# Kernel optimization log

Hardware: AMD Instinct MI355X
Metric: run time of the kernel (lower is better)

Reference implementation:

```python
import math
import jax, jax.numpy as jnp
import numpy as np

# ---- SLAYER neuron / simulation constants (from config) ----
THETA = 10.0      # spike threshold
TAU_SR = 10.0     # PSP (SRM) kernel time constant
TAU_REF = 1.0     # refractory kernel time constant
TS = 1.0          # simulation time step
T_SAMPLE = 500    # number of time bins
B, N_IN, N_HID, N_OUT = 64, 1024, 1024, 10


def _alpha_kernel(tau, mult, eps=0.01):
    """slayer _calculateAlphaKernel: mult * t/tau * exp(1 - t/tau), truncated."""
    vals = []
    t = 0.0
    while t < T_SAMPLE:
        v = mult * t / tau * math.exp(1.0 - t / tau)
        if abs(v) < eps and t > tau:
            break
        vals.append(v)
        t += TS
    return np.asarray(vals, np.float32)

SRM_KERNEL = jnp.asarray(_alpha_kernel(TAU_SR, 1.0))            # [K]
REF_KERNEL = jnp.asarray(_alpha_kernel(TAU_REF, -2.0 * THETA))  # [Kr], REF_KERNEL[0] == 0


def dense(x, W):
    # per-timestep fully-connected layer (slayer.dense == 1x1x1 conv3d, no bias)
    # x: [B, Nin, T], W: [Nout, Nin] -> [B, Nout, T]
    return jnp.einsum('oi,bit->bot', W, x)


def psp(x):
    # causal temporal convolution with the SRM kernel: out[t] = Ts * sum_k srm[k] * x[t-k]
    Bx, N, T = x.shape
    K = SRM_KERNEL.shape[0]
    k = SRM_KERNEL[::-1].reshape(1, 1, K).astype(x.dtype)  # flip -> true convolution
    y = jax.lax.conv_general_dilated(
        x.reshape(Bx * N, 1, T), k, (1,), [(K - 1, 0)],
        dimension_numbers=('NCH', 'OIH', 'NCH'))
    return y.reshape(Bx, N, T) * TS


def spike_impl(u_in):
    # sequential LIF thresholding with refractory feedback (slayer spike kernel)
    # u_in: [B, N, T] membrane drive; returns (spikes, membrane) both [B, N, T]
    Kr = REF_KERNEL.shape[0]
    # buf[j] is the refractory contribution arriving at step t+j; new spike at t
    # contributes REF_KERNEL[j] at t+j (REF_KERNEL[0]==0), i.e. shifted kernel into buf.
    refk = jnp.concatenate([REF_KERNEL[1:], jnp.zeros((1,), u_in.dtype)]).astype(u_in.dtype)
    buf0 = jnp.zeros(u_in.shape[:-1] + (Kr,), u_in.dtype)

    def step(buf, u_t):
        u = u_t + buf[..., 0]                              # membrane at time t
        s = (u >= THETA).astype(u_in.dtype) / TS           # spike (amplitude 1/Ts)
        buf = jnp.concatenate([buf[..., 1:], jnp.zeros_like(buf[..., :1])], axis=-1)
        buf = buf + s[..., None] * refk
        return buf, (s, u)

    _, (s, u) = jax.lax.scan(step, buf0, jnp.moveaxis(u_in, -1, 0))
    return jnp.moveaxis(s, 0, -1), jnp.moveaxis(u, 0, -1)


def setup_inputs() -> dict:
    key = jax.random.key(0)
    k1, k2, k3 = jax.random.split(key, 3)
    spike_input = (jax.random.uniform(k1, (B, N_IN, T_SAMPLE)) < 0.05).astype(jnp.float32)
    W1 = jax.random.normal(k2, (N_HID, N_IN), jnp.float32) * 0.3
    W2 = jax.random.normal(k3, (N_OUT, N_HID), jnp.float32) * 0.3
    return {"spike_input": spike_input, "W1": W1, "W2": W2}


def reference(spike_input, W1, W2):
    s1, _ = spike_impl(psp(dense(spike_input, W1)))
    s2, _ = spike_impl(psp(dense(s1, W2)))
    return s2
```

## Files before the change

kernel.cpp:

```cpp
#include <hip/hip_runtime.h>
#include <stdint.h>
#include <math.h>

#define T_SIM 500
#define NB    64
#define NIN   1024
#define NHID  1024
#define NOUT  10
#define KSRM  77
#define CHUNK 32
#define TT5   12
#define NT5   42
#define RINGN 104
#define NGW   16

__device__ __forceinline__ double srm_tap(int k) {
  double u = (double)k / 10.0;
  double v = u * exp(1.0 - u);
  return (double)(float)v;
}
__device__ __forceinline__ double ref_tap(int j) {
  double v = (-20.0 * (double)j) * exp(1.0 - (double)j);
  return (double)(float)v;
}

__global__ __launch_bounds__(64)
void k_pack(const float* __restrict__ x, unsigned long long* __restrict__ bits) {
  const int b = blockIdx.x, ig = blockIdx.y, tc = blockIdx.z;
  const int lane = threadIdx.x;
  const float* xr = x + ((size_t)b * NIN + ig * 64 + lane) * T_SIM;
  const int t0 = tc * 100;
  for (int t = t0; t < t0 + 100; t += 4) {
    const float4 v = *(const float4*)(xr + t);
    unsigned long long m0 = __ballot(v.x > 0.5f);
    unsigned long long m1 = __ballot(v.y > 0.5f);
    unsigned long long m2 = __ballot(v.z > 0.5f);
    unsigned long long m3 = __ballot(v.w > 0.5f);
    if (lane == 0) {
      unsigned long long* w = bits + (size_t)(b * T_SIM + t) * 16 + ig;
      w[0] = m0; w[16] = m1; w[32] = m2; w[48] = m3;
    }
  }
}

__global__ __launch_bounds__(256)
void k_transpose(const float* __restrict__ W1, float* __restrict__ W1T) {
  __shared__ float tile[64][65];
  const int bo = blockIdx.x * 64, bi = blockIdx.y * 64;
  for (int k = threadIdx.x; k < 4096; k += 256) {
    int r = k >> 6, c = k & 63;
    tile[r][c] = W1[(size_t)(bo + r) * NIN + bi + c];
  }
  __syncthreads();
  for (int k = threadIdx.x; k < 4096; k += 256) {
    int r = k >> 6, c = k & 63;
    W1T[(size_t)(bi + r) * NHID + bo + c] = tile[c][r];
  }
}

__global__ __launch_bounds__(128)
void k_dense1(const uint32_t* __restrict__ bits, const float* __restrict__ W1T,
              double* __restrict__ a1c, int col_base) {
  __shared__ int list[NIN];
  __shared__ int nact_s;
  const int col_loc = blockIdx.x;
  const int tid = threadIdx.x;
  if (tid < 32) {
    uint32_t w = bits[(size_t)(col_base + col_loc) * 32 + tid];
    int c = __popc(w);
    int p = c;
#pragma unroll
    for (int d = 1; d < 32; d <<= 1) {
      int q = __shfl_up(p, d);
      if (tid >= d) p += q;
    }
    int excl = p - c;
    while (w) {
      const int j = __ffs(w) - 1;
      w &= w - 1;
      list[excl++] = tid * 32 + j;
    }
    if (tid == 31) nact_s = excl;
  }
  __syncthreads();
  const int n = nact_s;
  const int o = blockIdx.y * 512 + tid * 4;
  double ax[4] = {0,0,0,0}, ay[4] = {0,0,0,0};
  double az[4] = {0,0,0,0}, aw[4] = {0,0,0,0};
  float4 L[8];
  int g = 0;
  if (n >= 8) {
#pragma unroll
    for (int r = 0; r < 8; ++r)
      L[r] = *(const float4*)(W1T + (size_t)list[r] * NHID + o);
    for (g = 0; g + 16 <= n; g += 8) {
      float4 Nb[8];
#pragma unroll
      for (int r = 0; r < 8; ++r)
        Nb[r] = *(const float4*)(W1T + (size_t)list[g + 8 + r] * NHID + o);
#pragma unroll
      for (int r = 0; r < 8; ++r) {
        const int s = r & 3;
        ax[s] += (double)L[r].x; ay[s] += (double)L[r].y;
        az[s] += (double)L[r].z; aw[s] += (double)L[r].w;
      }
#pragma unroll
      for (int r = 0; r < 8; ++r) L[r] = Nb[r];
    }
#pragma unroll
    for (int r = 0; r < 8; ++r) {
      const int s = r & 3;
      ax[s] += (double)L[r].x; ay[s] += (double)L[r].y;
      az[s] += (double)L[r].z; aw[s] += (double)L[r].w;
    }
    g += 8;
  }
  for (; g < n; ++g) {
    const float4 wv = *(const float4*)(W1T + (size_t)list[g] * NHID + o);
    const int s = g & 3;
    ax[s] += (double)wv.x; ay[s] += (double)wv.y;
    az[s] += (double)wv.z; aw[s] += (double)wv.w;
  }
  double* dst = a1c + (size_t)col_loc * NHID + o;
  __builtin_nontemporal_store((ax[0] + ax[1]) + (ax[2] + ax[3]), dst + 0);
  __builtin_nontemporal_store((ay[0] + ay[1]) + (ay[2] + ay[3]), dst + 1);
  __builtin_nontemporal_store((az[0] + az[1]) + (az[2] + az[3]), dst + 2);
  __builtin_nontemporal_store((aw[0] + aw[1]) + (aw[2] + aw[3]), dst + 3);
}

__global__ __launch_bounds__(256)
void k_ps1(const double* __restrict__ a1c, uint16_t* __restrict__ s1h,
           int b_base) {
  __shared__ double S[RINGN * NGW];
  __shared__ double Yp[2][4][TT5 * NGW];
  __shared__ double TB[80];
  const int ng = blockIdx.x, b_loc = blockIdx.y;
  const int tid = threadIdx.x;
  const double* __restrict__ abase = a1c + (size_t)b_loc * T_SIM * NHID + ng * NGW;
  uint16_t* __restrict__ sbase = s1h + (size_t)(b_base + b_loc) * T_SIM * 64 + ng;

  if (tid < 80) TB[tid] = (tid <= 76) ? srm_tap(tid) : 0.0;
  for (int i = tid; i < RINGN * NGW; i += 256) S[i] = 0.0;
  __syncthreads();
  for (int id = tid; id < TT5 * NGW; id += 256) {
    const int r = id >> 4, nn = id & 15;
    S[r * NGW + nn] = abase[(size_t)r * NHID + nn];
  }

  const bool isFIR = (tid < 192);
  const int g   = tid / 48;
  const int rem = tid - g * 48;
  const int q   = rem >> 4;
  const int n   = rem & 15;
  double tap[20];
  __syncthreads();
  if (isFIR) {
#pragma unroll
    for (int j = 0; j < 20; ++j) tap[j] = TB[20 * g + j];
  }
  double refk[11];
#pragma unroll
  for (int j = 1; j <= 10; ++j) refk[j] = ref_tap(j);
  uint32_t smask = 0;

  for (int k = 0; k < NT5; ++k) {
    const int t0 = k * TT5;
    const int tv = (T_SIM - t0 < TT5) ? (T_SIM - t0) : TT5;
    const int t0n = t0 + TT5;
    const int tvn = (t0n >= T_SIM) ? 0 : ((T_SIM - t0n < TT5) ? (T_SIM - t0n) : TT5);
    if (isFIR) {
      double pf = 0.0;
      const int pr = tid >> 4, pn = tid & 15;
      const bool hasPf = (tid < tvn * NGW);
      if (hasPf) pf = abase[(size_t)(t0n + pr) * NHID + pn];
      const int tb = t0 + q * 4;
      int slot = (tb - 20 * g - 19 + 10400) % RINGN;
      double a0 = 0, a1 = 0, a2 = 0, a3 = 0;
#pragma unroll
      for (int s = 0; s < 23; ++s) {
        const double v = S[slot * NGW + n];
        slot = slot + 1;
        if (slot == RINGN) slot = 0;
        if (s <= 19)           a0 += tap[19 - s] * v;
        if (s >= 1 && s <= 20) a1 += tap[20 - s] * v;
        if (s >= 2 && s <= 21) a2 += tap[21 - s] * v;
        if (s >= 3)            a3 += tap[22 - s] * v;
      }
      double* Yk = Yp[k & 1][g];
      const int tl = q * 4;
      if (tl + 0 < tv) Yk[(tl + 0) * NGW + n] = a0;
      if (tl + 1 < tv) Yk[(tl + 1) * NGW + n] = a1;
      if (tl + 2 < tv) Yk[(tl + 2) * NGW + n] = a2;
      if (tl + 3 < tv) Yk[(tl + 3) * NGW + n] = a3;
      if (hasPf) S[((t0n + pr) % RINGN) * NGW + pn] = pf;
    } else if (k > 0) {
      const int lane = tid - 192;
      if (lane < NGW) {
        const int t0p = t0 - TT5;
        const double* Y0 = Yp[(k - 1) & 1][0];
        const double* Y1 = Yp[(k - 1) & 1][1];
        const double* Y2 = Yp[(k - 1) & 1][2];
        const double* Y3 = Yp[(k - 1) & 1][3];
        for (int gg = 0; gg < TT5; ++gg) {
          double u = (Y0[gg * NGW + lane] + Y1[gg * NGW + lane]) +
                     (Y2[gg * NGW + lane] + Y3[gg * NGW + lane]);
#pragma unroll
          for (int j = 10; j >= 1; --j)
            u += refk[j] * (double)((smask >> (j - 1)) & 1u);
          const bool sp = (u >= 10.0);
          smask = (smask << 1) | (sp ? 1u : 0u);
          const unsigned long long bm = __ballot(sp);
          if (lane == 0) sbase[(size_t)(t0p + gg) * 64] = (uint16_t)bm;
        }
      }
    }
    __syncthreads();
  }
  if (!isFIR) {
    const int lane = tid - 192;
    if (lane < NGW) {
      const int t0p = (NT5 - 1) * TT5;
      const int tvp = T_SIM - t0p;
      const double* Y0 = Yp[(NT5 - 1) & 1][0];
      const double* Y1 = Yp[(NT5 - 1) & 1][1];
      const double* Y2 = Yp[(NT5 - 1) & 1][2];
      const double* Y3 = Yp[(NT5 - 1) & 1][3];
      for (int gg = 0; gg < tvp; ++gg) {
        double u = (Y0[gg * NGW + lane] + Y1[gg * NGW + lane]) +
                   (Y2[gg * NGW + lane] + Y3[gg * NGW + lane]);
#pragma unroll
        for (int j = 10; j >= 1; --j)
          u += refk[j] * (double)((smask >> (j - 1)) & 1u);
        const bool sp = (u >= 10.0);
        smask = (smask << 1) | (sp ? 1u : 0u);
        const unsigned long long bm = __ballot(sp);
        if (lane == 0) sbase[(size_t)(t0p + gg) * 64] = (uint16_t)bm;
      }
    }
  }
}

__global__ __launch_bounds__(256)
void k_dense2(const uint32_t* __restrict__ s1w,
              const float* __restrict__ W2, double* __restrict__ a2) {
  __shared__ float w2t[NHID * NOUT];
  for (int k = threadIdx.x; k < NHID * NOUT; k += 256) {
    const int o = k >> 10, i = k & 1023;
    w2t[i * NOUT + o] = W2[k];
  }
  __syncthreads();
  const int col = blockIdx.x * 256 + threadIdx.x;
  double acc[NOUT];
#pragma unroll
  for (int o = 0; o < NOUT; ++o) acc[o] = 0.0;
  const uint32_t* w = s1w + (size_t)col * 32;
  for (int wi = 0; wi < 32; ++wi) {
    uint32_t m = w[wi];
    const int ibase = wi * 32;
    while (m) {
      const int j = __ffs(m) - 1;
      m &= m - 1;
      const float* row = &w2t[(ibase + j) * NOUT];
#pragma unroll
      for (int o = 0; o < NOUT; ++o) acc[o] += (double)row[o];
    }
  }
  double* outp = a2 + (size_t)col * NOUT;
#pragma unroll
  for (int o = 0; o < NOUT; ++o) outp[o] = acc[o];
}

__global__ __launch_bounds__(256)
void k_l2(const double* __restrict__ a2, float* __restrict__ out) {
  __shared__ double S[T_SIM * NOUT];
  __shared__ double Y[T_SIM * NOUT];
  __shared__ double srm[KSRM];
  const int b = blockIdx.x, tid = threadIdx.x;
  if (tid < KSRM) srm[tid] = srm_tap(tid);
  for (int i = tid; i < T_SIM * NOUT; i += 256)
    S[i] = a2[(size_t)b * T_SIM * NOUT + i];
  __syncthreads();
  for (int i = tid; i < T_SIM * NOUT; i += 256) {
    const int t = i / 10, o = i - t * 10;
    const int kmax = (t < KSRM - 1) ? t : (KSRM - 1);
    double acc = 0.0;
    for (int k = 0; k <= kmax; ++k)
      acc += srm[k] * S[(t - k) * 10 + o];
    Y[i] = acc;
  }
  __syncthreads();
  if (tid < NOUT) {
    double refk[11];
#pragma unroll
    for (int j = 1; j <= 10; ++j) refk[j] = ref_tap(j);
    uint32_t smask = 0;
    float* op = out + ((size_t)b * NOUT + tid) * T_SIM;
    for (int t = 0; t < T_SIM; ++t) {
      double u = Y[t * 10 + tid];
#pragma unroll
      for (int j = 10; j >= 1; --j)
        u += refk[j] * (double)((smask >> (j - 1)) & 1u);
      const bool sp = (u >= 10.0);
      smask = (smask << 1) | (sp ? 1u : 0u);
      op[t] = sp ? 1.0f : 0.0f;
    }
  }
}

extern "C" void kernel_launch(void* const* d_in, const int* in_sizes, int n_in,
                              void* d_out, int out_size, void* d_ws, size_t ws_size,
                              hipStream_t stream) {
  const float* x  = (const float*)d_in[0];
  const float* W1 = (const float*)d_in[1];
  const float* W2 = (const float*)d_in[2];
  float* out = (float*)d_out;

  char* ws = (char*)d_ws;
  unsigned long long* bits1 = (unsigned long long*)(ws);
  float*  W1T = (float*) (ws + 4096000);
  double* a1c = (double*)(ws + 8290304);
  uint32_t* s1w = (uint32_t*)(ws + 139362304);
  double* a2  = (double*)(ws + 143458304);

  hipLaunchKernelGGL(k_pack, dim3(NB, 16, 5), dim3(64), 0, stream, x, bits1);
  hipLaunchKernelGGL(k_transpose, dim3(16, 16), dim3(256), 0, stream, W1, W1T);

  for (int bc = 0; bc < NB; bc += CHUNK) {
    hipLaunchKernelGGL(k_dense1, dim3(CHUNK * T_SIM, 2), dim3(128), 0, stream,
                       (const uint32_t*)bits1, W1T, a1c, bc * T_SIM);
    hipLaunchKernelGGL(k_ps1, dim3(64, CHUNK), dim3(256), 0, stream,
                       a1c, (uint16_t*)s1w, bc);
  }

  hipLaunchKernelGGL(k_dense2, dim3(125), dim3(256), 0, stream, s1w, W2, a2);
  hipLaunchKernelGGL(k_l2, dim3(NB), dim3(256), 0, stream, a2, out);
}
```

Baseline: 994.3 us.

## Split fused PSP+spike kernel into parallel FIR and separate spike scan

Replaces the fused layer-1 kernel, which overlapped a ring-buffer FIR with a 16-lane spike scan, with two kernels. The new FIR kernel tiles time into 64-step blocks across a 3D grid so every tile computes in parallel. The scan kernel then runs the sequential refractory threshold over 64 neurons per wave. Batch chunks shrink from 32 to 16 so the extra intermediate buffer fits. This raises parallelism in the FIR stage, but adds a full double-precision round trip through global memory and more launches.

```diff
diff --git a/kernel.cpp b/kernel.cpp
--- a/kernel.cpp
+++ b/kernel.cpp
@@ -8,11 +8,9 @@
 #define NHID  1024
 #define NOUT  10
 #define KSRM  77
-#define CHUNK 32
-#define TT5   12
-#define NT5   42
-#define RINGN 104
-#define NGW   16
+#define CHUNK 16
+#define FTT   64
+#define FSTG  140
 
 __device__ __forceinline__ double srm_tap(int k) {
   double u = (double)k / 10.0;
@@ -129,114 +127,65 @@
 }
 
 __global__ __launch_bounds__(256)
-void k_ps1(const double* __restrict__ a1c, uint16_t* __restrict__ s1h,
-           int b_base) {
-  __shared__ double S[RINGN * NGW];
-  __shared__ double Yp[2][4][TT5 * NGW];
+void k_fir(const double* __restrict__ a1c, double* __restrict__ Y) {
+  __shared__ double S[FSTG * 32];
   __shared__ double TB[80];
-  const int ng = blockIdx.x, b_loc = blockIdx.y;
+  const int tt = blockIdx.x;
+  const int ng = blockIdx.y;
+  const int b  = blockIdx.z;
   const int tid = threadIdx.x;
-  const double* __restrict__ abase = a1c + (size_t)b_loc * T_SIM * NHID + ng * NGW;
-  uint16_t* __restrict__ sbase = s1h + (size_t)(b_base + b_loc) * T_SIM * 64 + ng;
-
+  const int T0 = tt * FTT;
+  const double* __restrict__ abase = a1c + (size_t)b * T_SIM * NHID + ng * 32;
   if (tid < 80) TB[tid] = (tid <= 76) ? srm_tap(tid) : 0.0;
-  for (int i = tid; i < RINGN * NGW; i += 256) S[i] = 0.0;
-  __syncthreads();
-  for (int id = tid; id < TT5 * NGW; id += 256) {
-    const int r = id >> 4, nn = id & 15;
-    S[r * NGW + nn] = abase[(size_t)r * NHID + nn];
-  }
-
-  const bool isFIR = (tid < 192);
-  const int g   = tid / 48;
-  const int rem = tid - g * 48;
-  const int q   = rem >> 4;
-  const int n   = rem & 15;
-  double tap[20];
-  __syncthreads();
-  if (isFIR) {
-#pragma unroll
-    for (int j = 0; j < 20; ++j) tap[j] = TB[20 * g + j];
-  }
+  for (int e = tid; e < FSTG * 32; e += 256) {
+    const int r = e >> 5, n = e & 31;
+    const int t = T0 - 76 + r;
+    double v = 0.0;
+    if (t >= 0 && t < T_SIM) v = abase[(size_t)t * NHID + n];
+    S[r * 32 + n] = v;
+  }
+  __syncthreads();
+  const int n = tid & 31, tq = tid >> 5;
+  double acc[8] = {0, 0, 0, 0, 0, 0, 0, 0};
+  const int base = (tq * 8 + 76) * 32 + n;
+  for (int k = 0; k <= 76; ++k) {
+    const double tap = TB[k];
+    const double* Sp = &S[base - k * 32];
+#pragma unroll
+    for (int r = 0; r < 8; ++r)
+      acc[r] += tap * Sp[r * 32];
+  }
+  double* ybase = Y + (size_t)b * T_SIM * NHID + ng * 32 + n;
+  const int tb = T0 + tq * 8;
+#pragma unroll
+  for (int r = 0; r < 8; ++r)
+    if (tb + r < T_SIM)
+      __builtin_nontemporal_store(acc[r], &ybase[(size_t)(tb + r) * NHID]);
+}
+
+__global__ __launch_bounds__(64)
+void k_scan(const double* __restrict__ Y, uint32_t* __restrict__ s1w,
+            int b_base) {
+  const int n0 = blockIdx.x * 64;
+  const int b  = blockIdx.y;
+  const int lane = threadIdx.x;
+  const double* __restrict__ ybase = Y + (size_t)b * T_SIM * NHID + n0 + lane;
+  unsigned long long* __restrict__ sbase = (unsigned long long*)
+      (s1w + (size_t)(b_base + b) * T_SIM * 32 + (n0 >> 5));
   double refk[11];
 #pragma unroll
   for (int j = 1; j <= 10; ++j) refk[j] = ref_tap(j);
   uint32_t smask = 0;
-
-  for (int k = 0; k < NT5; ++k) {
-    const int t0 = k * TT5;
-    const int tv = (T_SIM - t0 < TT5) ? (T_SIM - t0) : TT5;
-    const int t0n = t0 + TT5;
-    const int tvn = (t0n >= T_SIM) ? 0 : ((T_SIM - t0n < TT5) ? (T_SIM - t0n) : TT5);
-    if (isFIR) {
-      double pf = 0.0;
-      const int pr = tid >> 4, pn = tid & 15;
-      const bool hasPf = (tid < tvn * NGW);
-      if (hasPf) pf = abase[(size_t)(t0n + pr) * NHID + pn];
-      const int tb = t0 + q * 4;
-      int slot = (tb - 20 * g - 19 + 10400) % RINGN;
-      double a0 = 0, a1 = 0, a2 = 0, a3 = 0;
-#pragma unroll
-      for (int s = 0; s < 23; ++s) {
-        const double v = S[slot * NGW + n];
-        slot = slot + 1;
-        if (slot == RINGN) slot = 0;
-        if (s <= 19)           a0 += tap[19 - s] * v;
-        if (s >= 1 && s <= 20) a1 += tap[20 - s] * v;
-        if (s >= 2 && s <= 21) a2 += tap[21 - s] * v;
-        if (s >= 3)            a3 += tap[22 - s] * v;
-      }
-      double* Yk = Yp[k & 1][g];
-      const int tl = q * 4;
-      if (tl + 0 < tv) Yk[(tl + 0) * NGW + n] = a0;
-      if (tl + 1 < tv) Yk[(tl + 1) * NGW + n] = a1;
-      if (tl + 2 < tv) Yk[(tl + 2) * NGW + n] = a2;
-      if (tl + 3 < tv) Yk[(tl + 3) * NGW + n] = a3;
-      if (hasPf) S[((t0n + pr) % RINGN) * NGW + pn] = pf;
-    } else if (k > 0) {
-      const int lane = tid - 192;
-      if (lane < NGW) {
-        const int t0p = t0 - TT5;
-        const double* Y0 = Yp[(k - 1) & 1][0];
-        const double* Y1 = Yp[(k - 1) & 1][1];
-        const double* Y2 = Yp[(k - 1) & 1][2];
-        const double* Y3 = Yp[(k - 1) & 1][3];
-        for (int gg = 0; gg < TT5; ++gg) {
-          double u = (Y0[gg * NGW + lane] + Y1[gg * NGW + lane]) +
-                     (Y2[gg * NGW + lane] + Y3[gg * NGW + lane]);
-#pragma unroll
-          for (int j = 10; j >= 1; --j)
-            u += refk[j] * (double)((smask >> (j - 1)) & 1u);
-          const bool sp = (u >= 10.0);
-          smask = (smask << 1) | (sp ? 1u : 0u);
-          const unsigned long long bm = __ballot(sp);
-          if (lane == 0) sbase[(size_t)(t0p + gg) * 64] = (uint16_t)bm;
-        }
-      }
-    }
-    __syncthreads();
-  }
-  if (!isFIR) {
-    const int lane = tid - 192;
-    if (lane < NGW) {
-      const int t0p = (NT5 - 1) * TT5;
-      const int tvp = T_SIM - t0p;
-      const double* Y0 = Yp[(NT5 - 1) & 1][0];
-      const double* Y1 = Yp[(NT5 - 1) & 1][1];
-      const double* Y2 = Yp[(NT5 - 1) & 1][2];
-      const double* Y3 = Yp[(NT5 - 1) & 1][3];
-      for (int gg = 0; gg < tvp; ++gg) {
-        double u = (Y0[gg * NGW + lane] + Y1[gg * NGW + lane]) +
-                   (Y2[gg * NGW + lane] + Y3[gg * NGW + lane]);
-#pragma unroll
-        for (int j = 10; j >= 1; --j)
-          u += refk[j] * (double)((smask >> (j - 1)) & 1u);
-        const bool sp = (u >= 10.0);
-        smask = (smask << 1) | (sp ? 1u : 0u);
-        const unsigned long long bm = __ballot(sp);
-        if (lane == 0) sbase[(size_t)(t0p + gg) * 64] = (uint16_t)bm;
-      }
-    }
+#pragma unroll 4
+  for (int t = 0; t < T_SIM; ++t) {
+    double u = ybase[(size_t)t * NHID];
+#pragma unroll
+    for (int j = 10; j >= 1; --j)
+      u += refk[j] * (double)((smask >> (j - 1)) & 1u);
+    const bool sp = (u >= 10.0);
+    smask = (smask << 1) | (sp ? 1u : 0u);
+    const unsigned long long bm = __ballot(sp);
+    if (lane == 0) sbase[(size_t)t * 16] = bm;
   }
 }
 
@@ -317,19 +266,22 @@
 
   char* ws = (char*)d_ws;
   unsigned long long* bits1 = (unsigned long long*)(ws);
-  float*  W1T = (float*) (ws + 4096000);
+  float*  W1T = (float*)(ws + 4096000);
   double* a1c = (double*)(ws + 8290304);
+  double* Yb  = (double*)(ws + 73826304);
   uint32_t* s1w = (uint32_t*)(ws + 139362304);
   double* a2  = (double*)(ws + 143458304);
 
   hipLaunchKernelGGL(k_pack, dim3(NB, 16, 5), dim3(64), 0, stream, x, bits1);
   hipLaunchKernelGGL(k_transpose, dim3(16, 16), dim3(256), 0, stream, W1, W1T);
 
-  for (int bc = 0; bc < NB; bc += CHUNK) {
+  for (int c = 0; c < NB / CHUNK; ++c) {
     hipLaunchKernelGGL(k_dense1, dim3(CHUNK * T_SIM, 2), dim3(128), 0, stream,
-                       (const uint32_t*)bits1, W1T, a1c, bc * T_SIM);
-    hipLaunchKernelGGL(k_ps1, dim3(64, CHUNK), dim3(256), 0, stream,
-                       a1c, (uint16_t*)s1w, bc);
+                       (const uint32_t*)bits1, W1T, a1c, c * CHUNK * T_SIM);
+    hipLaunchKernelGGL(k_fir, dim3(8, 32, CHUNK), dim3(256), 0, stream,
+                       a1c, Yb);
+    hipLaunchKernelGGL(k_scan, dim3(16, CHUNK), dim3(64), 0, stream,
+                       Yb, s1w, c * CHUNK);
   }
 
   hipLaunchKernelGGL(k_dense2, dim3(125), dim3(256), 0, stream, s1w, W2, a2);
```

Result: slower. 1.758 ms (+76.8%).
